# Optimization experiments

Measured on AMD Instinct MI355X. Metric: run time of the kernel, lower is better.

Reference implementation:

```python
import jax, jax.numpy as jnp
import numpy as np

N_NODES = 100000
N_EDGES = 1600000
N_GRAPHS = 64
IN_DIM = 256
OUT_DIM = 512
H1 = OUT_DIM // 4   # 128
H2 = OUT_DIM // 2   # 256


def glorot(key, shape):
    lim = float(np.sqrt(6.0 / (shape[0] + shape[1])))
    return jax.random.uniform(key, shape, jnp.float32, -lim, lim)


def setup_inputs() -> dict:
    key = jax.random.key(0)
    ks = jax.random.split(key, 8)
    x = jax.random.normal(ks[0], (N_NODES, IN_DIM), jnp.float32)
    edge_index = jax.random.randint(ks[1], (2, N_EDGES), 0, N_NODES, jnp.int64)
    batch = jnp.sort(jax.random.randint(ks[2], (N_NODES,), 0, N_GRAPHS, jnp.int64))
    return {
        'x': x,
        'edge_index': edge_index,
        'batch': batch,
        'W1': glorot(ks[3], (IN_DIM, H1)),
        'b1': jnp.zeros((H1,), jnp.float32),
        'W2': glorot(ks[4], (H1, H2)),
        'b2': jnp.zeros((H2,), jnp.float32),
        'fc_W': glorot(ks[5], (H2, OUT_DIM)),
        'fc_b': jnp.zeros((OUT_DIM,), jnp.float32),
    }


def gcn_conv(x, W, b, src, dst, n_nodes):
    # PyG GCNConv (default): add self-loops, sym-normalized aggregation of XW + bias
    h = x @ W                                   # [N, F_out] transform first (cheaper gather)
    ones = jnp.ones((src.shape[0],), h.dtype)
    deg = jax.ops.segment_sum(ones, dst, num_segments=n_nodes)  # includes self-loops
    dinv = jax.lax.rsqrt(jnp.maximum(deg, 1.0))
    norm = dinv[src] * dinv[dst]                # [E]
    msg = h[src] * norm[:, None]                # gather + scale
    out = jax.ops.segment_sum(msg, dst, num_segments=n_nodes)   # scatter-add
    return out + b


def reference(x, edge_index, batch, W1, b1, W2, b2, fc_W, fc_b):
    n = x.shape[0]
    loops = jnp.arange(n, dtype=edge_index.dtype)
    src = jnp.concatenate([edge_index[0], loops])
    dst = jnp.concatenate([edge_index[1], loops])

    h = jax.nn.relu(gcn_conv(x, W1, b1, src, dst, n))   # dropout = identity (eval)
    h = jax.nn.relu(gcn_conv(h, W2, b2, src, dst, n))

    # global_mean_pool over batch ids
    sums = jax.ops.segment_sum(h, batch, num_segments=N_GRAPHS)
    cnts = jax.ops.segment_sum(jnp.ones((n,), h.dtype), batch, num_segments=N_GRAPHS)
    pooled = sums / jnp.maximum(cnts, 1.0)[:, None]     # [B, H2]

    return jax.nn.relu(pooled @ fc_W + fc_b)            # [B, OUT_DIM]
```

## Files before the change

### kernel.cpp

```cpp
#include <hip/hip_runtime.h>
#include <hip/hip_bf16.h>
#include <cstdint>

#define N_NODES 100000
#define N_EDGES 1600000
#define N_GRAPHS 64
#define IN_DIM 256
#define HD1 128
#define HD2 256
#define OUT_DIM 512

#define NBUCK 196
#define NBLK  196
#define EPB   8192

typedef __bf16 bf16x8 __attribute__((ext_vector_type(8)));
typedef float f32x4 __attribute__((ext_vector_type(4)));

static __device__ __forceinline__ float bflo(uint32_t v) { return __uint_as_float(v << 16); }
static __device__ __forceinline__ float bfhi(uint32_t v) { return __uint_as_float(v & 0xffff0000u); }
static __device__ __forceinline__ uint32_t f2bf_bits(float f) {
    uint32_t u = __float_as_uint(f);
    return (u + 0x7fffu + ((u >> 16) & 1u)) >> 16;
}
static __device__ __forceinline__ uint32_t packbf(float a, float b) {
    return f2bf_bits(a) | (f2bf_bits(b) << 16);
}
static __device__ __forceinline__ float bf2f(uint16_t b) { return __uint_as_float(((uint32_t)b) << 16); }

__global__ void k_probe(const uint32_t* __restrict__ xw, const int* __restrict__ ei,
                        int* __restrict__ flags) {
    if (threadIdx.x != 0 || blockIdx.x != 0) return;
    int mid = 0;
    for (int i = 0; i < 64; i++) {
        uint32_t f = (xw[i] >> 23) & 0xFF;
        if (f >= 64 && f < 200) mid++;
    }
    flags[0] = (mid < 32) ? 1 : 0;
    int nz = 0;
    for (int i = 0; i < 64; i++) if (ei[2 * i + 1] != 0) nz++;
    flags[1] = (nz == 0) ? 1 : 0;
}

static __device__ __forceinline__ int ld_idx(const int* p, int i, int sh) { return p[i << sh]; }
static __device__ __forceinline__ float ld_f(const void* p, int i, int isbf) {
    return isbf ? bf2f(((const uint16_t*)p)[i]) : ((const float*)p)[i];
}

__global__ __launch_bounds__(256) void k_prep(const void* __restrict__ W1, const void* __restrict__ W2,
                                              const void* __restrict__ fcW, const void* __restrict__ b1,
                                              const void* __restrict__ b2, const void* __restrict__ fcb,
                                              uint16_t* __restrict__ W1T, uint16_t* __restrict__ W2T,
                                              uint16_t* __restrict__ fcWc, uint16_t* __restrict__ bc1,
                                              uint16_t* __restrict__ bc2, uint16_t* __restrict__ fcbc,
                                              const int* __restrict__ flags) {
    int i = blockIdx.x * 256 + threadIdx.x;
    int isbf = flags[0];
    if (i < 32768) {
        int n = i / IN_DIM, k = i % IN_DIM;
        W1T[i] = (uint16_t)f2bf_bits(ld_f(W1, k * HD1 + n, isbf));
    } else if (i < 65536) {
        int j = i - 32768;
        int n = j / HD1, k = j % HD1;
        W2T[j] = (uint16_t)f2bf_bits(ld_f(W2, k * HD2 + n, isbf));
    } else if (i < 196608) {
        int j = i - 65536;
        fcWc[j] = (uint16_t)f2bf_bits(ld_f(fcW, j, isbf));
    } else if (i < 196736) {
        bc1[i - 196608] = (uint16_t)f2bf_bits(ld_f(b1, i - 196608, isbf));
    } else if (i < 196992) {
        bc2[i - 196736] = (uint16_t)f2bf_bits(ld_f(b2, i - 196736, isbf));
    } else if (i < 197504) {
        fcbc[i - 196992] = (uint16_t)f2bf_bits(ld_f(fcb, i - 196992, isbf));
    }
}


__global__ __launch_bounds__(256) void k_hist(const int* __restrict__ ei, int* __restrict__ bh,
                                              const int* __restrict__ flags) {
    __shared__ int h[NBUCK];
    int t = threadIdx.x, blk = blockIdx.x;
    if (t < NBUCK) h[t] = 0;
    __syncthreads();
    int sh = flags[1];
    int base = blk * EPB;
#pragma unroll
    for (int k = 0; k < EPB / 256; k++) {
        int e = base + k * 256 + t;
        if (e < N_EDGES) atomicAdd(&h[ld_idx(ei, N_EDGES + e, sh) >> 9], 1);
    }
    __syncthreads();
    if (t < NBUCK) bh[blk * NBUCK + t] = h[t];
}

__global__ __launch_bounds__(256) void k_colscan(const int* __restrict__ bh, int* __restrict__ bhoff,
                                                 int* __restrict__ bucket_cnt) {
    __shared__ int s[256];
    int b = blockIdx.x, t = threadIdx.x;
    int v = (t < NBLK) ? bh[t * NBUCK + b] : 0;
    s[t] = v; __syncthreads();
    for (int off = 1; off < 256; off <<= 1) {
        int x = (t >= off) ? s[t - off] : 0;
        __syncthreads();
        s[t] += x;
        __syncthreads();
    }
    if (t < NBLK) bhoff[t * NBUCK + b] = s[t] - v;
    if (t == 255) bucket_cnt[b] = s[255];
}

__global__ __launch_bounds__(256) void k_bscan(const int* __restrict__ bucket_cnt,
                                               int* __restrict__ bucket_base,
                                               int* __restrict__ row_ptr) {
    __shared__ int s[256];
    int t = threadIdx.x;
    int v = (t < NBUCK) ? bucket_cnt[t] : 0;
    s[t] = v; __syncthreads();
    for (int off = 1; off < 256; off <<= 1) {
        int x = (t >= off) ? s[t - off] : 0;
        __syncthreads();
        s[t] += x;
        __syncthreads();
    }
    if (t < NBUCK) bucket_base[t] = s[t] - v;
    if (t == NBUCK - 1) { bucket_base[NBUCK] = s[t]; row_ptr[N_NODES] = s[t]; }
}

__global__ __launch_bounds__(256) void k_part(const int* __restrict__ ei,
                                              const int* __restrict__ bucket_base,
                                              const int* __restrict__ bhoff,
                                              int* __restrict__ tmp,
                                              const int* __restrict__ flags) {
    __shared__ int cur[NBUCK];
    int t = threadIdx.x, blk = blockIdx.x;
    if (t < NBUCK) cur[t] = bucket_base[t] + bhoff[blk * NBUCK + t];
    __syncthreads();
    int sh = flags[1];
    int base = blk * EPB;
#pragma unroll
    for (int k = 0; k < EPB / 256; k++) {
        int e = base + k * 256 + t;
        if (e < N_EDGES) {
            int s = ld_idx(ei, e, sh), d = ld_idx(ei, N_EDGES + e, sh);
            int pos = atomicAdd(&cur[d >> 9], 1);
            tmp[pos] = (s << 9) | (d & 511);
        }
    }
}

__global__ __launch_bounds__(256) void k_bsort(const int* __restrict__ tmp,
                                               const int* __restrict__ bucket_base,
                                               int* __restrict__ csr_src,
                                               int* __restrict__ row_ptr,
                                               float* __restrict__ dinv) {
    __shared__ int h[512], a[512], c[512];
    int b = blockIdx.x, t = threadIdx.x;
    int beg = bucket_base[b], end = bucket_base[b + 1];
    h[t] = 0; h[t + 256] = 0;
    __syncthreads();
    for (int i = beg + t; i < end; i += 256) atomicAdd(&h[tmp[i] & 511], 1);
    __syncthreads();
    a[t] = h[t]; a[t + 256] = h[t + 256];
    __syncthreads();
    for (int off = 1; off < 512; off <<= 1) {
        int x0 = (t >= off) ? a[t - off] : 0;
        int x1 = ((t + 256) >= off) ? a[t + 256 - off] : 0;
        __syncthreads();
        a[t] += x0; a[t + 256] += x1;
        __syncthreads();
    }
#pragma unroll
    for (int u = 0; u < 2; u++) {
        int i = t + u * 256;
        int node = (b << 9) + i;
        int ex = a[i] - h[i];
        if (node < N_NODES) {
            row_ptr[node] = beg + ex;
            dinv[node] = rsqrtf((float)(h[i] + 1));
        }
        c[i] = ex;
    }
    __syncthreads();
    for (int i = beg + t; i < end; i += 256) {
        int e = tmp[i];
        int pos = atomicAdd(&c[e & 511], 1);
        csr_src[beg + pos] = e >> 9;
    }
}

#define GCNT_CHUNK 8
__global__ __launch_bounds__(256) void k_gcnt(const int* __restrict__ bat, int* __restrict__ gcnt,
                                              const int* __restrict__ flags) {
    __shared__ int h[N_GRAPHS];
    int t = threadIdx.x;
    if (t < N_GRAPHS) h[t] = 0;
    __syncthreads();
    int sh = flags[1];
    int base = (blockIdx.x * 256 + t) * GCNT_CHUNK;
    int cur = -1, run = 0;
#pragma unroll
    for (int u = 0; u < GCNT_CHUNK; u++) {
        int i = base + u;
        if (i < N_NODES) {
            int g = ld_idx(bat, i, sh);
            if (g == cur) run++;
            else { if (run) atomicAdd(&h[cur], run); cur = g; run = 1; }
        }
    }
    if (run) atomicAdd(&h[cur], run);
    __syncthreads();
    if (t < N_GRAPHS) { int v = h[t]; if (v) atomicAdd(&gcnt[t], v); }
}


__global__ __launch_bounds__(256, 3) void k_gemm1(const void* __restrict__ Ain,
                                                  const uint16_t* __restrict__ BT,
                                                  uint16_t* __restrict__ C,
                                                  const int* __restrict__ flags) {
    const int M = N_NODES, K = IN_DIM, N = HD1;
    int isbf = flags[0];
    int t = threadIdx.x;
    int wave = t >> 6, lane = t & 63;
    int quad = lane >> 4, l16 = lane & 15;
    int m0 = blockIdx.x * 128 + wave * 32;

    f32x4 acc[2][8];
#pragma unroll
    for (int a = 0; a < 2; a++)
#pragma unroll
        for (int b = 0; b < 8; b++) acc[a][b] = f32x4{0.f, 0.f, 0.f, 0.f};

    int arow[2];
#pragma unroll
    for (int mt = 0; mt < 2; mt++) {
        int r = m0 + mt * 16 + l16;
        arow[mt] = r < M ? r : M - 1;
    }

#pragma unroll
    for (int ks = 0; ks < 8; ks++) {
        int kc = ks * 32 + quad * 8;
        bf16x8 af[2];
#pragma unroll
        for (int mt = 0; mt < 2; mt++) {
            int off = arow[mt] * K + kc;
            if (isbf) {
                af[mt] = *(const bf16x8*)((const uint16_t*)Ain + off);
            } else {
                const float* p = (const float*)Ain + off;
                f32x4 f0 = *(const f32x4*)p, f1 = *(const f32x4*)(p + 4);
                union { uint16_t u[8]; bf16x8 v; } r;
#pragma unroll
                for (int j = 0; j < 4; j++) {
                    r.u[j]     = (uint16_t)f2bf_bits(f0[j]);
                    r.u[4 + j] = (uint16_t)f2bf_bits(f1[j]);
                }
                af[mt] = r.v;
            }
        }
        bf16x8 bq[8];
#pragma unroll
        for (int nt = 0; nt < 8; nt++)
            bq[nt] = *(const bf16x8*)(BT + (nt * 16 + l16) * K + kc);
#pragma unroll
        for (int mt = 0; mt < 2; mt++)
#pragma unroll
            for (int nt = 0; nt < 8; nt++)
                acc[mt][nt] = __builtin_amdgcn_mfma_f32_16x16x32_bf16(af[mt], bq[nt], acc[mt][nt], 0, 0, 0);
    }

#pragma unroll
    for (int mt = 0; mt < 2; mt++)
#pragma unroll
        for (int reg = 0; reg < 4; reg++) {
            int row = m0 + mt * 16 + quad * 4 + reg;
            if (row < M)
#pragma unroll
                for (int nt = 0; nt < 8; nt++)
                    C[row * N + nt * 16 + l16] = (uint16_t)f2bf_bits(acc[mt][nt][reg]);
        }
}


template <int WITH_BIAS_RELU>
__global__ __launch_bounds__(256) void k_agg(const uint16_t* __restrict__ Yin, uint16_t* __restrict__ Yout,
                                             const int* __restrict__ row_ptr, const int* __restrict__ csr_src,
                                             const float* __restrict__ dinv, const uint16_t* __restrict__ bias) {
    int node = blockIdx.x * 4 + (threadIdx.x >> 6);
    int l = threadIdx.x & 63;
    const uint32_t* Y32 = (const uint32_t*)Yin;

    float wd = dinv[node];
    uint32_t v = Y32[(size_t)node * 64 + l];
    float a0 = wd * bflo(v), a1 = wd * bfhi(v);

    int e0 = row_ptr[node], e1 = row_ptr[node + 1];
    for (int cb = e0; cb < e1; cb += 64) {
        int cnt = e1 - cb; if (cnt > 64) cnt = 64;
        int my_src = 0; uint32_t my_w = 0;
        if (l < cnt) { my_src = csr_src[cb + l]; my_w = __float_as_uint(dinv[my_src]); }
        int rounds = (cnt + 15) >> 4;
        for (int r = 0; r < rounds; r++) {
            int jb = r * 16;
            uint32_t vv[16];
#pragma unroll
            for (int t = 0; t < 16; t++) {
                int s = __builtin_amdgcn_readlane(my_src, jb + t);
                vv[t] = Y32[(size_t)s * 64 + l];
            }
#pragma unroll
            for (int t = 0; t < 16; t++) {
                float w = __uint_as_float(__builtin_amdgcn_readlane(my_w, jb + t));
                a0 += w * bflo(vv[t]);
                a1 += w * bfhi(vv[t]);
            }
        }
    }
    a0 *= wd; a1 *= wd;
    if (WITH_BIAS_RELU) {
        a0 = fmaxf(a0 + bf2f(bias[2 * l]), 0.f);
        a1 = fmaxf(a1 + bf2f(bias[2 * l + 1]), 0.f);
    }
    ((uint32_t*)Yout)[(size_t)node * 64 + l] = packbf(a0, a1);
}


__global__ __launch_bounds__(256, 3) void k_gemm2_pool(const uint16_t* __restrict__ A,
                                                       const uint16_t* __restrict__ BT,
                                                       const uint16_t* __restrict__ bias,
                                                       const int* __restrict__ bat,
                                                       const int* __restrict__ flags,
                                                       float* __restrict__ pooled) {
    const int M = N_NODES, K = HD1;
    int t = threadIdx.x;
    int wave = t >> 6, lane = t & 63;
    int quad = lane >> 4, l16 = lane & 15;
    int m0 = blockIdx.x * 128 + wave * 32;
    int n0 = blockIdx.y * 128;

    f32x4 acc[2][8];
#pragma unroll
    for (int a = 0; a < 2; a++)
#pragma unroll
        for (int b = 0; b < 8; b++) acc[a][b] = f32x4{0.f, 0.f, 0.f, 0.f};

    int arow[2];
#pragma unroll
    for (int mt = 0; mt < 2; mt++) {
        int r = m0 + mt * 16 + l16;
        arow[mt] = r < M ? r : M - 1;
    }

#pragma unroll
    for (int ks = 0; ks < 4; ks++) {
        int kc = ks * 32 + quad * 8;
        bf16x8 af[2];
#pragma unroll
        for (int mt = 0; mt < 2; mt++)
            af[mt] = *(const bf16x8*)(A + arow[mt] * K + kc);
        bf16x8 bq[8];
#pragma unroll
        for (int nt = 0; nt < 8; nt++)
            bq[nt] = *(const bf16x8*)(BT + (n0 + nt * 16 + l16) * K + kc);
#pragma unroll
        for (int mt = 0; mt < 2; mt++)
#pragma unroll
            for (int nt = 0; nt < 8; nt++)
                acc[mt][nt] = __builtin_amdgcn_mfma_f32_16x16x32_bf16(af[mt], bq[nt], acc[mt][nt], 0, 0, 0);
    }

    int sh = flags[1];
    float bv[8];
#pragma unroll
    for (int nt = 0; nt < 8; nt++) bv[nt] = bf2f(bias[n0 + nt * 16 + l16]);

    if (m0 < M) {
        int gfirst = ld_idx(bat, m0, sh);
        int glast  = ld_idx(bat, m0 + 31, sh);
        if (gfirst == glast) {
#pragma unroll
            for (int nt = 0; nt < 8; nt++) {
                float s = 0.f;
#pragma unroll
                for (int mt = 0; mt < 2; mt++)
#pragma unroll
                    for (int reg = 0; reg < 4; reg++)
                        s += fmaxf(acc[mt][nt][reg] + bv[nt], 0.f);
                s += __shfl_xor(s, 16);
                s += __shfl_xor(s, 32);
                if (quad == 0)
                    atomicAdd(&pooled[gfirst * HD2 + n0 + nt * 16 + l16], s);
            }
        } else {
#pragma unroll
            for (int mt = 0; mt < 2; mt++) {
                int rb = m0 + mt * 16 + quad * 4;
#pragma unroll
                for (int reg = 0; reg < 4; reg++) {
                    int g = ld_idx(bat, rb + reg, sh);
#pragma unroll
                    for (int nt = 0; nt < 8; nt++)
                        atomicAdd(&pooled[g * HD2 + n0 + nt * 16 + l16],
                                  fmaxf(acc[mt][nt][reg] + bv[nt], 0.f));
                }
            }
        }
    }
}


__global__ __launch_bounds__(512) void k_final(const float* __restrict__ pooled, const int* __restrict__ gcnt,
                                               const uint16_t* __restrict__ fcWc, const uint16_t* __restrict__ fcbc,
                                               void* __restrict__ out, const int* __restrict__ flags) {
    __shared__ float pm[HD2];
    int g = blockIdx.x, t = threadIdx.x;
    if (t < HD2) pm[t] = pooled[g * HD2 + t] / fmaxf((float)gcnt[g], 1.0f);
    __syncthreads();
    float acc = bf2f(fcbc[t]);
    for (int k = 0; k < HD2; k++) acc = fmaf(pm[k], bf2f(fcWc[k * OUT_DIM + t]), acc);
    acc = fmaxf(acc, 0.f);
    if (flags[0]) ((uint16_t*)out)[g * OUT_DIM + t] = (uint16_t)f2bf_bits(acc);
    else          ((float*)out)[g * OUT_DIM + t] = acc;
}


extern "C" void kernel_launch(void* const* d_in, const int* in_sizes, int n_in,
                              void* d_out, int out_size, void* d_ws, size_t ws_size,
                              hipStream_t stream) {
    const void* x   = d_in[0];
    const int*  ei  = (const int*)d_in[1];
    const int*  bat = (const int*)d_in[2];
    const void* W1  = d_in[3];
    const void* b1  = d_in[4];
    const void* W2  = d_in[5];
    const void* b2  = d_in[6];
    const void* fcW = d_in[7];
    const void* fcb = d_in[8];

    char* ws = (char*)d_ws;
    size_t off = 0;
    auto alloc = [&](size_t bytes) -> void* {
        void* p = ws + off;
        off += (bytes + 255) & ~(size_t)255;
        return p;
    };
    uint16_t* buf0 = (uint16_t*)alloc((size_t)N_NODES * HD1 * 2);
    uint16_t* Hb   = (uint16_t*)alloc((size_t)N_NODES * HD1 * 2);
    int*   row_ptr = (int*)alloc((N_NODES + 1) * 4);
    int*   csr_src = (int*)alloc((size_t)N_EDGES * 4);
    int*   tmp     = (int*)alloc((size_t)N_EDGES * 4);
    int*   bh      = (int*)alloc(NBLK * NBUCK * 4);
    int*   bhoff   = (int*)alloc(NBLK * NBUCK * 4);
    int*   bucket_cnt  = (int*)alloc(NBUCK * 4);
    int*   bucket_base = (int*)alloc((NBUCK + 1) * 4);
    float* dinv    = (float*)alloc(N_NODES * 4);
    int*   gcnt    = (int*)alloc(N_GRAPHS * 4);
    float* pooled  = (float*)alloc(N_GRAPHS * HD2 * 4);
    uint16_t* W1T  = (uint16_t*)alloc(IN_DIM * HD1 * 2);
    uint16_t* W2T  = (uint16_t*)alloc(HD1 * HD2 * 2);
    uint16_t* bc1  = (uint16_t*)alloc(HD1 * 2);
    uint16_t* bc2  = (uint16_t*)alloc(HD2 * 2);
    uint16_t* fcWc = (uint16_t*)alloc(HD2 * OUT_DIM * 2);
    uint16_t* fcbc = (uint16_t*)alloc(OUT_DIM * 2);
    int*   flags   = (int*)alloc(64 * 4);

    uint16_t* Y1 = buf0;
    uint16_t* Zb = buf0;

    hipMemsetAsync(gcnt, 0, N_GRAPHS * 4, stream);
    hipMemsetAsync(pooled, 0, N_GRAPHS * HD2 * 4, stream);

    k_probe<<<1, 64, 0, stream>>>((const uint32_t*)x, ei, flags);

    k_prep<<<(197504 + 255) / 256, 256, 0, stream>>>(W1, W2, fcW, b1, b2, fcb,
                                                     W1T, W2T, fcWc, bc1, bc2, fcbc, flags);

    k_hist<<<NBLK, 256, 0, stream>>>(ei, bh, flags);
    k_colscan<<<NBUCK, 256, 0, stream>>>(bh, bhoff, bucket_cnt);
    k_bscan<<<1, 256, 0, stream>>>(bucket_cnt, bucket_base, row_ptr);
    k_part<<<NBLK, 256, 0, stream>>>(ei, bucket_base, bhoff, tmp, flags);
    k_bsort<<<NBUCK, 256, 0, stream>>>(tmp, bucket_base, csr_src, row_ptr, dinv);

    k_gcnt<<<(N_NODES + 256 * GCNT_CHUNK - 1) / (256 * GCNT_CHUNK), 256, 0, stream>>>(bat, gcnt, flags);

    k_gemm1<<<(N_NODES + 127) / 128, 256, 0, stream>>>(x, W1T, Y1, flags);
    k_agg<1><<<N_NODES / 4, 256, 0, stream>>>(Y1, Hb, row_ptr, csr_src, dinv, bc1);

    k_agg<0><<<N_NODES / 4, 256, 0, stream>>>(Hb, Zb, row_ptr, csr_src, dinv, nullptr);
    k_gemm2_pool<<<dim3((N_NODES + 127) / 128, 2), 256, 0, stream>>>(Zb, W2T, bc2, bat, flags, pooled);

    k_final<<<N_GRAPHS, 512, 0, stream>>>(pooled, gcnt, fcWc, fcbc, d_out, flags);
}
```

Baseline: 454.1 us.

## Retile GEMM kernels so waves split N and keep weights in registers

Both GEMM kernels are restructured so each block handles 32 rows and each wave owns a 32-column slice of the output. The wave loads its weight slice into registers once, so the per-k-step B loads from global memory go away. The A rows are shared across waves through cache rather than each wave reading its own rows. gemm2_pool now uses a single 512-thread block covering all 256 output columns instead of a 2D grid. This gives more, smaller blocks and fewer MFMAs per wave, and adds more pooled atomics per row tile. Bounds checks are dropped because N_NODES divides by 32.

Measured after the change: 479.3 us. +5.6%, slower.

```diff
diff --git a/kernel.cpp b/kernel.cpp
--- a/kernel.cpp
+++ b/kernel.cpp
@@ -213,29 +213,32 @@
 }
 
 
-__global__ __launch_bounds__(256, 3) void k_gemm1(const void* __restrict__ Ain,
+__global__ __launch_bounds__(256, 4) void k_gemm1(const void* __restrict__ Ain,
                                                   const uint16_t* __restrict__ BT,
                                                   uint16_t* __restrict__ C,
                                                   const int* __restrict__ flags) {
-    const int M = N_NODES, K = IN_DIM, N = HD1;
+    const int K = IN_DIM, N = HD1;
     int isbf = flags[0];
     int t = threadIdx.x;
     int wave = t >> 6, lane = t & 63;
     int quad = lane >> 4, l16 = lane & 15;
-    int m0 = blockIdx.x * 128 + wave * 32;
-
-    f32x4 acc[2][8];
+    int m0 = blockIdx.x * 32;
+    int n0 = wave * 32;
+
+    bf16x8 Bf[2][8];
+#pragma unroll
+    for (int nt = 0; nt < 2; nt++)
+#pragma unroll
+        for (int ks = 0; ks < 8; ks++)
+            Bf[nt][ks] = *(const bf16x8*)(BT + (n0 + nt * 16 + l16) * K + ks * 32 + quad * 8);
+
+    f32x4 acc[2][2];
 #pragma unroll
     for (int a = 0; a < 2; a++)
 #pragma unroll
-        for (int b = 0; b < 8; b++) acc[a][b] = f32x4{0.f, 0.f, 0.f, 0.f};
-
-    int arow[2];
-#pragma unroll
-    for (int mt = 0; mt < 2; mt++) {
-        int r = m0 + mt * 16 + l16;
-        arow[mt] = r < M ? r : M - 1;
-    }
+        for (int b = 0; b < 2; b++) acc[a][b] = f32x4{0.f, 0.f, 0.f, 0.f};
+
+    int arow[2] = { m0 + l16, m0 + 16 + l16 };
 
 #pragma unroll
     for (int ks = 0; ks < 8; ks++) {
@@ -258,15 +261,11 @@
                 af[mt] = r.v;
             }
         }
-        bf16x8 bq[8];
-#pragma unroll
-        for (int nt = 0; nt < 8; nt++)
-            bq[nt] = *(const bf16x8*)(BT + (nt * 16 + l16) * K + kc);
 #pragma unroll
         for (int mt = 0; mt < 2; mt++)
 #pragma unroll
-            for (int nt = 0; nt < 8; nt++)
-                acc[mt][nt] = __builtin_amdgcn_mfma_f32_16x16x32_bf16(af[mt], bq[nt], acc[mt][nt], 0, 0, 0);
+            for (int nt = 0; nt < 2; nt++)
+                acc[mt][nt] = __builtin_amdgcn_mfma_f32_16x16x32_bf16(af[mt], Bf[nt][ks], acc[mt][nt], 0, 0, 0);
     }
 
 #pragma unroll
@@ -274,10 +273,9 @@
 #pragma unroll
         for (int reg = 0; reg < 4; reg++) {
             int row = m0 + mt * 16 + quad * 4 + reg;
-            if (row < M)
-#pragma unroll
-                for (int nt = 0; nt < 8; nt++)
-                    C[row * N + nt * 16 + l16] = (uint16_t)f2bf_bits(acc[mt][nt][reg]);
+#pragma unroll
+            for (int nt = 0; nt < 2; nt++)
+                C[row * N + n0 + nt * 16 + l16] = (uint16_t)f2bf_bits(acc[mt][nt][reg]);
         }
 }
 
@@ -325,31 +323,33 @@
 }
 
 
-__global__ __launch_bounds__(256, 3) void k_gemm2_pool(const uint16_t* __restrict__ A,
+__global__ __launch_bounds__(512, 4) void k_gemm2_pool(const uint16_t* __restrict__ A,
                                                        const uint16_t* __restrict__ BT,
                                                        const uint16_t* __restrict__ bias,
                                                        const int* __restrict__ bat,
                                                        const int* __restrict__ flags,
                                                        float* __restrict__ pooled) {
-    const int M = N_NODES, K = HD1;
+    const int K = HD1;
     int t = threadIdx.x;
     int wave = t >> 6, lane = t & 63;
     int quad = lane >> 4, l16 = lane & 15;
-    int m0 = blockIdx.x * 128 + wave * 32;
-    int n0 = blockIdx.y * 128;
-
-    f32x4 acc[2][8];
+    int m0 = blockIdx.x * 32;
+    int n0 = wave * 32;
+
+    bf16x8 Bf[2][4];
+#pragma unroll
+    for (int nt = 0; nt < 2; nt++)
+#pragma unroll
+        for (int ks = 0; ks < 4; ks++)
+            Bf[nt][ks] = *(const bf16x8*)(BT + (n0 + nt * 16 + l16) * K + ks * 32 + quad * 8);
+
+    f32x4 acc[2][2];
 #pragma unroll
     for (int a = 0; a < 2; a++)
 #pragma unroll
-        for (int b = 0; b < 8; b++) acc[a][b] = f32x4{0.f, 0.f, 0.f, 0.f};
-
-    int arow[2];
-#pragma unroll
-    for (int mt = 0; mt < 2; mt++) {
-        int r = m0 + mt * 16 + l16;
-        arow[mt] = r < M ? r : M - 1;
-    }
+        for (int b = 0; b < 2; b++) acc[a][b] = f32x4{0.f, 0.f, 0.f, 0.f};
+
+    int arow[2] = { m0 + l16, m0 + 16 + l16 };
 
 #pragma unroll
     for (int ks = 0; ks < 4; ks++) {
@@ -358,51 +358,45 @@
 #pragma unroll
         for (int mt = 0; mt < 2; mt++)
             af[mt] = *(const bf16x8*)(A + arow[mt] * K + kc);
-        bf16x8 bq[8];
-#pragma unroll
-        for (int nt = 0; nt < 8; nt++)
-            bq[nt] = *(const bf16x8*)(BT + (n0 + nt * 16 + l16) * K + kc);
 #pragma unroll
         for (int mt = 0; mt < 2; mt++)
 #pragma unroll
-            for (int nt = 0; nt < 8; nt++)
-                acc[mt][nt] = __builtin_amdgcn_mfma_f32_16x16x32_bf16(af[mt], bq[nt], acc[mt][nt], 0, 0, 0);
+            for (int nt = 0; nt < 2; nt++)
+                acc[mt][nt] = __builtin_amdgcn_mfma_f32_16x16x32_bf16(af[mt], Bf[nt][ks], acc[mt][nt], 0, 0, 0);
     }
 
     int sh = flags[1];
-    float bv[8];
-#pragma unroll
-    for (int nt = 0; nt < 8; nt++) bv[nt] = bf2f(bias[n0 + nt * 16 + l16]);
-
-    if (m0 < M) {
-        int gfirst = ld_idx(bat, m0, sh);
-        int glast  = ld_idx(bat, m0 + 31, sh);
-        if (gfirst == glast) {
-#pragma unroll
-            for (int nt = 0; nt < 8; nt++) {
-                float s = 0.f;
-#pragma unroll
-                for (int mt = 0; mt < 2; mt++)
-#pragma unroll
-                    for (int reg = 0; reg < 4; reg++)
-                        s += fmaxf(acc[mt][nt][reg] + bv[nt], 0.f);
-                s += __shfl_xor(s, 16);
-                s += __shfl_xor(s, 32);
-                if (quad == 0)
-                    atomicAdd(&pooled[gfirst * HD2 + n0 + nt * 16 + l16], s);
-            }
-        } else {
-#pragma unroll
-            for (int mt = 0; mt < 2; mt++) {
-                int rb = m0 + mt * 16 + quad * 4;
-#pragma unroll
-                for (int reg = 0; reg < 4; reg++) {
-                    int g = ld_idx(bat, rb + reg, sh);
-#pragma unroll
-                    for (int nt = 0; nt < 8; nt++)
-                        atomicAdd(&pooled[g * HD2 + n0 + nt * 16 + l16],
-                                  fmaxf(acc[mt][nt][reg] + bv[nt], 0.f));
-                }
+    float bv[2];
+#pragma unroll
+    for (int nt = 0; nt < 2; nt++) bv[nt] = bf2f(bias[n0 + nt * 16 + l16]);
+
+    int gfirst = ld_idx(bat, m0, sh);
+    int glast  = ld_idx(bat, m0 + 31, sh);
+    if (gfirst == glast) {
+#pragma unroll
+        for (int nt = 0; nt < 2; nt++) {
+            float s = 0.f;
+#pragma unroll
+            for (int mt = 0; mt < 2; mt++)
+#pragma unroll
+                for (int reg = 0; reg < 4; reg++)
+                    s += fmaxf(acc[mt][nt][reg] + bv[nt], 0.f);
+            s += __shfl_xor(s, 16);
+            s += __shfl_xor(s, 32);
+            if (quad == 0)
+                atomicAdd(&pooled[gfirst * HD2 + n0 + nt * 16 + l16], s);
+        }
+    } else {
+#pragma unroll
+        for (int mt = 0; mt < 2; mt++) {
+            int rb = m0 + mt * 16 + quad * 4;
+#pragma unroll
+            for (int reg = 0; reg < 4; reg++) {
+                int g = ld_idx(bat, rb + reg, sh);
+#pragma unroll
+                for (int nt = 0; nt < 2; nt++)
+                    atomicAdd(&pooled[g * HD2 + n0 + nt * 16 + l16],
+                              fmaxf(acc[mt][nt][reg] + bv[nt], 0.f));
             }
         }
     }
@@ -483,11 +477,11 @@
 
     k_gcnt<<<(N_NODES + 256 * GCNT_CHUNK - 1) / (256 * GCNT_CHUNK), 256, 0, stream>>>(bat, gcnt, flags);
 
-    k_gemm1<<<(N_NODES + 127) / 128, 256, 0, stream>>>(x, W1T, Y1, flags);
+    k_gemm1<<<N_NODES / 32, 256, 0, stream>>>(x, W1T, Y1, flags);
     k_agg<1><<<N_NODES / 4, 256, 0, stream>>>(Y1, Hb, row_ptr, csr_src, dinv, bc1);
 
     k_agg<0><<<N_NODES / 4, 256, 0, stream>>>(Hb, Zb, row_ptr, csr_src, dinv, nullptr);
-    k_gemm2_pool<<<dim3((N_NODES + 127) / 128, 2), 256, 0, stream>>>(Zb, W2T, bc2, bat, flags, pooled);
+    k_gemm2_pool<<<N_NODES / 32, 512, 0, stream>>>(Zb, W2T, bc2, bat, flags, pooled);
 
     k_final<<<N_GRAPHS, 512, 0, stream>>>(pooled, gcnt, fcWc, fcbc, d_out, flags);
 }
```
